# Performance work log

Measured on AMD Instinct MI355X. Metric: run time of the kernel, lower is better.

Reference implementation:

```python
import jax, jax.numpy as jnp
import numpy as np

INF = 1.0e6  # 'infinity' for squared EDT; max real value is ~3*128^2 ~ 5e4


def edt_1d_sq(f, axis):
    """One pass of Felzenszwalb separable squared EDT along `axis`.
    d[i] = min_j f[j] + (i - j)^2  (brute-force vectorized lower envelope)."""
    f = jnp.moveaxis(f, axis, -1)
    n = f.shape[-1]
    i = jnp.arange(n, dtype=f.dtype)
    sq = (i[:, None] - i[None, :]) ** 2  # (n, n)
    d = jnp.min(f[..., None, :] + sq, axis=-1)  # (..., n)
    return jnp.moveaxis(d, -1, axis)


def compute_fg_dtm(mask):
    """Euclidean distance transform of foreground (distance to nearest background),
    matching scipy.ndimage.distance_transform_edt applied per batch element on the
    (C, X, Y, Z) mask (C==1 so the channel axis pass is the identity).
    mask: bool (B, 1, X, Y, Z) -> float32 (B, 1, X, Y, Z)."""
    def per_b(m):
        g = jnp.where(m, jnp.float32(INF), jnp.float32(0.0))
        for ax in range(m.ndim):
            g = edt_1d_sq(g, ax)
        return jnp.sqrt(g)
    return jax.lax.map(per_b, mask)


def setup_inputs() -> dict:
    key = jax.random.key(0)
    k1, k2, k3 = jax.random.split(key, 3)
    B, C, X, Y, Z = 2, 2, 128, 128, 128
    return {
        "outputs": jax.random.normal(k1, (B, C, X, Y, Z), dtype=jnp.float32),
        "outputs_dist": jax.random.normal(k2, (B, C, X, Y, Z), dtype=jnp.float32) * 10.0,
        "y": jax.random.randint(k3, (B, 1, X, Y, Z), 0, 2),
        "distance_map_weight": 1.0,
    }


def reference(outputs, outputs_dist, y, distance_map_weight):
    n_pred_ch = outputs.shape[1]
    # MONAI one_hot: (B,1,X,Y,Z) int labels -> (B,C,X,Y,Z) float
    y1h = jnp.moveaxis(jax.nn.one_hot(y[:, 0], n_pred_ch, dtype=outputs.dtype), -1, 1)
    x = outputs[:, 1:]            # foreground logits (B, 1, X, Y, Z)
    t = y1h[:, 1:]                # foreground mask
    od = outputs_dist[:, 1:]
    gt_dis = compute_fg_dtm(t > 0.5)
    # BCE with logits (mean reduction), numerically stable
    loss_ce = jnp.mean(jnp.maximum(x, 0.0) - x * t + jnp.log1p(jnp.exp(-jnp.abs(x))))
    # dice loss, flattened per batch element
    N = x.shape[0]
    smooth = jnp.float32(1.0)
    p = jax.nn.sigmoid(x).reshape(N, -1)
    tf = t.reshape(N, -1)
    dice = (2.0 * jnp.sum(p * tf, axis=1) + smooth) / (jnp.sum(p, axis=1) + jnp.sum(tf, axis=1) + smooth)
    loss_dice = 1.0 - jnp.sum(dice) / N
    # weighted L1 on the distance head, masked by the foreground mask
    msum = jnp.sum(t)
    loss_dist = jnp.where(
        msum == 0,
        jnp.float32(0.0),
        jnp.sum(jnp.abs(od - gt_dis) * t) / jnp.maximum(msum, jnp.float32(1e-12)),
    )
    return loss_ce + loss_dice + distance_map_weight * loss_dist
```

## Files before the change

### kernel.cpp

```cpp
#include <hip/hip_runtime.h>
#include <math.h>

#define M_SPATIAL 2097152

__device__ __forceinline__ float wave_redf(float v) {
#pragma unroll
  for (int o = 32; o > 0; o >>= 1) v += __shfl_down(v, o, 64);
  return v;
}
__device__ __forceinline__ double wave_redd(double v) {
#pragma unroll
  for (int o = 32; o > 0; o >>= 1) v += __shfl_down(v, o, 64);
  return v;
}


__global__ __launch_bounds__(256) void kAB(const int* __restrict__ y,
                                           const float* __restrict__ outputs,
                                           float* __restrict__ g,
                                           double* __restrict__ part) {
  int blk = blockIdx.x;
  int b  = blk >> 9;
  int yy = (blk >> 2) & 127;
  int zq = blk & 3;
  int t  = threadIdx.x;
  int c  = t >> 5;
  int zl = t & 31;
  int x0 = c * 16;
  size_t sp   = (size_t)yy * 128 + (size_t)zq * 32 + zl;
  size_t base = (size_t)b * M_SPATIAL + sp;
  const float* xc = outputs + (size_t)(b * 2 + 1) * M_SPATIAL;

  int yb[16];
  float xv[16];
#pragma unroll
  for (int k = 0; k < 16; ++k) yb[k] = y[base + (size_t)(x0 + k) * 16384];
#pragma unroll
  for (int k = 0; k < 16; ++k) xv[k] = xc[sp + (size_t)(x0 + k) * 16384];

  int lastE = -200, nextE = 400;
#pragma unroll
  for (int k = 0; k < 16; ++k) lastE = (yb[k] == 1) ? lastE : (x0 + k);
#pragma unroll
  for (int k = 15; k >= 0; --k) nextE = (yb[k] == 1) ? nextE : (x0 + k);

  __shared__ int lE[8][32];
  __shared__ int nE[8][32];
  lE[c][zl] = lastE;
  nE[c][zl] = nextE;
  __syncthreads();

  int carryL = -200, carryN = 400;
#pragma unroll
  for (int q = 0; q < 7; ++q) {
    if (q < c)     carryL = max(carryL, lE[q][zl]);
    if (q + 1 > c) carryN = min(carryN, nE[q + 1][zl]);
  }

  float yy2f = (float)(yy * yy);
  float hinf = 1000000.f + yy2f;

  int df[16];
  int ll = carryL;
#pragma unroll
  for (int k = 0; k < 16; ++k) {
    ll = (yb[k] == 1) ? ll : (x0 + k);
    df[k] = min(x0 + k - ll, 200);
  }
  float ov[16];
  int nn = carryN;
#pragma unroll
  for (int k = 15; k >= 0; --k) {
    nn = (yb[k] == 1) ? nn : (x0 + k);
    int m = min(df[k], min(nn - (x0 + k), 200));
    ov[k] = (m >= 128) ? hinf : ((float)(m * m) + yy2f);
  }
#pragma unroll
  for (int k = 0; k < 16; ++k) g[base + (size_t)(x0 + k) * 16384] = ov[k];

  float ce = 0.f, ps = 0.f, pts = 0.f, tsum = 0.f;
#pragma unroll
  for (int k = 0; k < 16; ++k) {
    float tt = (yb[k] == 1) ? 1.0f : 0.0f;
    float xx = xv[k];
    ce += fmaxf(xx, 0.0f) - xx * tt + log1pf(expf(-fabsf(xx)));
    float p = 1.0f / (1.0f + expf(-xx));
    ps += p; pts += p * tt; tsum += tt;
  }
  float r0 = wave_redf(ce), r1 = wave_redf(ps), r2 = wave_redf(pts), r3 = wave_redf(tsum);
  __shared__ float sm[4][4];
  int lane = t & 63, w = t >> 6;
  if (lane == 0) { sm[w][0] = r0; sm[w][1] = r1; sm[w][2] = r2; sm[w][3] = r3; }
  __syncthreads();
  if (t == 0) {
    part[blk]        = (double)(sm[0][0] + sm[1][0] + sm[2][0] + sm[3][0]);
    part[1024 + blk] = (double)(sm[0][1] + sm[1][1] + sm[2][1] + sm[3][1]);
    part[2048 + blk] = (double)(sm[0][2] + sm[1][2] + sm[2][2] + sm[3][2]);
    part[3072 + blk] = (double)(sm[0][3] + sm[1][3] + sm[2][3] + sm[3][3]);
  }
}

__global__ __launch_bounds__(512) void kCD(const float* __restrict__ g,
                                           const float* __restrict__ od,
                                           double* __restrict__ part) {
  __shared__ float sbuf[128 * 132];
  __shared__ float sred[8];
  int blk = blockIdx.x;
  int b = blk >> 7, xx = blk & 127;
  int t = threadIdx.x;
  size_t rb = (size_t)b * M_SPATIAL + (size_t)xx * 16384;

  const float4* g4 = (const float4*)(g + rb);
#pragma unroll
  for (int r = 0; r < 8; ++r) {
    int i4 = t + r * 512;
    float4 v = g4[i4];
    int flat = i4 * 4;
    int ys = flat >> 7, zs = flat & 127;
    *(float4*)&sbuf[ys * 132 + zs] = v;
  }
  __syncthreads();

  {
    int z = t & 127, ibase = (t >> 7) * 32;
    float zq = (float)(z * z);
    float best[32], mc[32];
#pragma unroll
    for (int k = 0; k < 32; ++k) {
      best[k] = 3.0e38f;
      mc[k] = -2.0f * (float)(ibase + k);
    }
#pragma unroll 2
    for (int j = 0; j < 128; j += 2) {
      float h0 = sbuf[j * 132 + z];
      float h1 = sbuf[(j + 1) * 132 + z];
      float j0 = (float)j, j1 = (float)(j + 1);
#pragma unroll
      for (int k = 0; k < 32; ++k)
        best[k] = fminf(fminf(fmaf(mc[k], j0, h0), fmaf(mc[k], j1, h1)), best[k]);
    }
    __syncthreads();
#pragma unroll
    for (int k = 0; k < 32; ++k) {
      int i = ibase + k;
      float dY = (float)(i * i) + best[k];
      sbuf[z * 129 + i] = dY + zq;
    }
  }
  __syncthreads();

  int yl = t >> 2, izb = (t & 3) * 32;
  size_t odb = (size_t)(2 * b + 1) * M_SPATIAL + (size_t)xx * 16384 +
               (size_t)yl * 128 + (size_t)izb;
  const float4* o4 = (const float4*)(od + odb);
  float4 ovv[8];
#pragma unroll
  for (int r = 0; r < 8; ++r) ovv[r] = o4[r];

  float best[32], mc[32];
#pragma unroll
  for (int k = 0; k < 32; ++k) {
    best[k] = 3.0e38f;
    mc[k] = -2.0f * (float)(izb + k);
  }
#pragma unroll 2
  for (int j = 0; j < 128; j += 2) {
    float h0 = sbuf[j * 129 + yl];
    float h1 = sbuf[(j + 1) * 129 + yl];
    float j0 = (float)j, j1 = (float)(j + 1);
#pragma unroll
    for (int k = 0; k < 32; ++k)
      best[k] = fminf(fminf(fmaf(mc[k], j0, h0), fmaf(mc[k], j1, h1)), best[k]);
  }
  const float* of = (const float*)ovv;
  float dist = 0.f;
#pragma unroll
  for (int k = 0; k < 32; ++k) {
    int i = izb + k;
    float dv = (float)(i * i) + best[k];
    if (dv > 0.f) dist += fabsf(of[k] - sqrtf(dv));
  }
  float r = wave_redf(dist);
  int lane = t & 63, w = t >> 6;
  if (lane == 0) sred[w] = r;
  __syncthreads();
  if (t == 0) {
    float s = 0.f;
#pragma unroll
    for (int q = 0; q < 8; ++q) s += sred[q];
    part[4096 + blk] = (double)s;
  }
}

__global__ __launch_bounds__(256) void k_final(const double* __restrict__ part,
                                               const float* __restrict__ wptr,
                                               float* __restrict__ out) {
  int i = threadIdx.x;
  double ce  = part[i] + part[i + 256] + part[i + 512] + part[i + 768];
  double p0  = part[1024 + i] + part[1024 + i + 256];
  double p1  = part[1536 + i] + part[1536 + i + 256];
  double pt0 = part[2048 + i] + part[2048 + i + 256];
  double pt1 = part[2560 + i] + part[2560 + i + 256];
  double t0  = part[3072 + i] + part[3072 + i + 256];
  double t1  = part[3584 + i] + part[3584 + i + 256];
  double ds  = part[4096 + i];

  ce = wave_redd(ce); p0 = wave_redd(p0); p1 = wave_redd(p1);
  pt0 = wave_redd(pt0); pt1 = wave_redd(pt1);
  t0 = wave_redd(t0); t1 = wave_redd(t1); ds = wave_redd(ds);

  __shared__ double sm[4][8];
  int lane = threadIdx.x & 63, w = threadIdx.x >> 6;
  if (lane == 0) {
    sm[w][0] = ce; sm[w][1] = p0; sm[w][2] = p1; sm[w][3] = pt0;
    sm[w][4] = pt1; sm[w][5] = t0; sm[w][6] = t1; sm[w][7] = ds;
  }
  __syncthreads();
  if (threadIdx.x == 0) {
    double a[8];
    for (int q = 0; q < 8; ++q) a[q] = sm[0][q] + sm[1][q] + sm[2][q] + sm[3][q];
    double cem = a[0] / 4194304.0;
    double dice0 = (2.0 * a[3] + 1.0) / (a[1] + a[5] + 1.0);
    double dice1 = (2.0 * a[4] + 1.0) / (a[2] + a[6] + 1.0);
    double ldice = 1.0 - 0.5 * (dice0 + dice1);
    double msum = a[5] + a[6];
    double ldist = (msum == 0.0) ? 0.0 : a[7] / fmax(msum, 1e-12);
    out[0] = (float)(cem + ldice + (double)wptr[0] * ldist);
  }
}

extern "C" void kernel_launch(void* const* d_in, const int* in_sizes, int n_in,
                              void* d_out, int out_size, void* d_ws, size_t ws_size,
                              hipStream_t stream) {
  const float* outputs      = (const float*)d_in[0];
  const float* outputs_dist = (const float*)d_in[1];
  const int*   y            = (const int*)d_in[2];
  const float* wptr         = (const float*)d_in[3];
  float* out = (float*)d_out;

  double* part = (double*)d_ws;
  float* g = (float*)((char*)d_ws + 65536);

  kAB<<<1024, 256, 0, stream>>>(y, outputs, g, part);
  kCD<<<256, 512, 0, stream>>>(g, outputs_dist, part);
  k_final<<<1, 256, 0, stream>>>(part, wptr, out);
}
```

Measured before the change: 160.2 us.

## Double kCD threads, use packed FMA and v_min3 in brute-force EDT passes

The Y and Z lower-envelope passes in kCD now run with 1024 threads per block, each handling 16 outputs instead of 32. The inner loop computes two candidates with a packed 2-wide FMA and merges them into the running minimum with an inline-asm v_min3_f32. The outputs_dist loads are issued at kernel start so they overlap the shared-memory fill and first pass. This aims to raise occupancy and cut VALU instruction count per candidate, at the cost of a larger block size, possible register pressure, and reliance on inline asm.

```diff
diff --git a/kernel.cpp b/kernel.cpp
--- a/kernel.cpp
+++ b/kernel.cpp
@@ -3,6 +3,8 @@
 
 #define M_SPATIAL 2097152
 
+typedef float f32x2 __attribute__((ext_vector_type(2)));
+
 __device__ __forceinline__ float wave_redf(float v) {
 #pragma unroll
   for (int o = 32; o > 0; o >>= 1) v += __shfl_down(v, o, 64);
@@ -12,6 +14,11 @@
 #pragma unroll
   for (int o = 32; o > 0; o >>= 1) v += __shfl_down(v, o, 64);
   return v;
+}
+__device__ __forceinline__ float min3f(float a, float b, float c) {
+  float d;
+  asm("v_min3_f32 %0, %1, %2, %3" : "=v"(d) : "v"(a), "v"(b), "v"(c));
+  return d;
 }
 
 
@@ -100,20 +107,28 @@
   }
 }
 
-__global__ __launch_bounds__(512) void kCD(const float* __restrict__ g,
-                                           const float* __restrict__ od,
-                                           double* __restrict__ part) {
+__global__ __launch_bounds__(1024) void kCD(const float* __restrict__ g,
+                                            const float* __restrict__ od,
+                                            double* __restrict__ part) {
   __shared__ float sbuf[128 * 132];
-  __shared__ float sred[8];
+  __shared__ float sred[16];
   int blk = blockIdx.x;
   int b = blk >> 7, xx = blk & 127;
   int t = threadIdx.x;
   size_t rb = (size_t)b * M_SPATIAL + (size_t)xx * 16384;
 
+  int yl = t >> 3, izb = (t & 7) * 16;
+  size_t odb = (size_t)(2 * b + 1) * M_SPATIAL + (size_t)xx * 16384 +
+               (size_t)yl * 128 + (size_t)izb;
+  const float4* o4 = (const float4*)(od + odb);
+  float4 ovv[4];
+#pragma unroll
+  for (int r = 0; r < 4; ++r) ovv[r] = o4[r];
+
   const float4* g4 = (const float4*)(g + rb);
 #pragma unroll
-  for (int r = 0; r < 8; ++r) {
-    int i4 = t + r * 512;
+  for (int r = 0; r < 4; ++r) {
+    int i4 = t + r * 1024;
     float4 v = g4[i4];
     int flat = i4 * 4;
     int ys = flat >> 7, zs = flat & 127;
@@ -122,26 +137,30 @@
   __syncthreads();
 
   {
-    int z = t & 127, ibase = (t >> 7) * 32;
+    int z = t & 127, ibase = (t >> 7) * 16;
     float zq = (float)(z * z);
-    float best[32], mc[32];
-#pragma unroll
-    for (int k = 0; k < 32; ++k) {
+    float best[16];
+    f32x2 mc2[16];
+#pragma unroll
+    for (int k = 0; k < 16; ++k) {
       best[k] = 3.0e38f;
-      mc[k] = -2.0f * (float)(ibase + k);
-    }
-#pragma unroll 2
+      float m = -2.0f * (float)(ibase + k);
+      mc2[k] = (f32x2){m, m};
+    }
+    f32x2 jv = {0.0f, 1.0f};
+#pragma unroll 4
     for (int j = 0; j < 128; j += 2) {
-      float h0 = sbuf[j * 132 + z];
-      float h1 = sbuf[(j + 1) * 132 + z];
-      float j0 = (float)j, j1 = (float)(j + 1);
-#pragma unroll
-      for (int k = 0; k < 32; ++k)
-        best[k] = fminf(fminf(fmaf(mc[k], j0, h0), fmaf(mc[k], j1, h1)), best[k]);
+      f32x2 hv = {sbuf[j * 132 + z], sbuf[(j + 1) * 132 + z]};
+#pragma unroll
+      for (int k = 0; k < 16; ++k) {
+        f32x2 v = __builtin_elementwise_fma(mc2[k], jv, hv);
+        best[k] = min3f(v.x, v.y, best[k]);
+      }
+      jv += (f32x2){2.0f, 2.0f};
     }
     __syncthreads();
 #pragma unroll
-    for (int k = 0; k < 32; ++k) {
+    for (int k = 0; k < 16; ++k) {
       int i = ibase + k;
       float dY = (float)(i * i) + best[k];
       sbuf[z * 129 + i] = dY + zq;
@@ -149,45 +168,43 @@
   }
   __syncthreads();
 
-  int yl = t >> 2, izb = (t & 3) * 32;
-  size_t odb = (size_t)(2 * b + 1) * M_SPATIAL + (size_t)xx * 16384 +
-               (size_t)yl * 128 + (size_t)izb;
-  const float4* o4 = (const float4*)(od + odb);
-  float4 ovv[8];
-#pragma unroll
-  for (int r = 0; r < 8; ++r) ovv[r] = o4[r];
-
-  float best[32], mc[32];
-#pragma unroll
-  for (int k = 0; k < 32; ++k) {
-    best[k] = 3.0e38f;
-    mc[k] = -2.0f * (float)(izb + k);
-  }
-#pragma unroll 2
-  for (int j = 0; j < 128; j += 2) {
-    float h0 = sbuf[j * 129 + yl];
-    float h1 = sbuf[(j + 1) * 129 + yl];
-    float j0 = (float)j, j1 = (float)(j + 1);
-#pragma unroll
-    for (int k = 0; k < 32; ++k)
-      best[k] = fminf(fminf(fmaf(mc[k], j0, h0), fmaf(mc[k], j1, h1)), best[k]);
-  }
-  const float* of = (const float*)ovv;
-  float dist = 0.f;
-#pragma unroll
-  for (int k = 0; k < 32; ++k) {
-    int i = izb + k;
-    float dv = (float)(i * i) + best[k];
-    if (dv > 0.f) dist += fabsf(of[k] - sqrtf(dv));
-  }
-  float r = wave_redf(dist);
-  int lane = t & 63, w = t >> 6;
-  if (lane == 0) sred[w] = r;
+  {
+    float best[16];
+    f32x2 mc2[16];
+#pragma unroll
+    for (int k = 0; k < 16; ++k) {
+      best[k] = 3.0e38f;
+      float m = -2.0f * (float)(izb + k);
+      mc2[k] = (f32x2){m, m};
+    }
+    f32x2 jv = {0.0f, 1.0f};
+#pragma unroll 4
+    for (int j = 0; j < 128; j += 2) {
+      f32x2 hv = {sbuf[j * 129 + yl], sbuf[(j + 1) * 129 + yl]};
+#pragma unroll
+      for (int k = 0; k < 16; ++k) {
+        f32x2 v = __builtin_elementwise_fma(mc2[k], jv, hv);
+        best[k] = min3f(v.x, v.y, best[k]);
+      }
+      jv += (f32x2){2.0f, 2.0f};
+    }
+    const float* of = (const float*)ovv;
+    float dist = 0.f;
+#pragma unroll
+    for (int k = 0; k < 16; ++k) {
+      int i = izb + k;
+      float dv = (float)(i * i) + best[k];
+      if (dv > 0.f) dist += fabsf(of[k] - sqrtf(dv));
+    }
+    float r = wave_redf(dist);
+    int lane = t & 63, w = t >> 6;
+    if (lane == 0) sred[w] = r;
+  }
   __syncthreads();
   if (t == 0) {
     float s = 0.f;
 #pragma unroll
-    for (int q = 0; q < 8; ++q) s += sred[q];
+    for (int q = 0; q < 16; ++q) s += sred[q];
     part[4096 + blk] = (double)s;
   }
 }
@@ -242,6 +259,6 @@
   float* g = (float*)((char*)d_ws + 65536);
 
   kAB<<<1024, 256, 0, stream>>>(y, outputs, g, part);
-  kCD<<<256, 512, 0, stream>>>(g, outputs_dist, part);
+  kCD<<<256, 1024, 0, stream>>>(g, outputs_dist, part);
   k_final<<<1, 256, 0, stream>>>(part, wptr, out);
 }
```

New measurement: 164.5 us. +2.7%, slower.
